# Kernel tuning notes

Measured on AMD Instinct MI355X. Metric: run time of the kernel, lower is better.

Reference implementation:

```python
import jax, jax.numpy as jnp
import numpy as np

H, W = 4096, 4096
KH, KW = 16, 16


def setup_inputs() -> dict:
    key = jax.random.key(0)
    kx, kw = jax.random.split(key)
    x = jax.random.normal(kx, (H, W), dtype=jnp.float32)
    weight = jax.random.normal(kw, (KH, KW), dtype=jnp.float32)
    bias = jnp.zeros((1,), dtype=jnp.float32)
    return {"x": x, "weight": weight, "bias": bias}


def reference(x, weight, bias):
    # 2D valid cross-correlation (no kernel flip), single channel, + scalar bias.
    # lax.conv_general_dilated computes cross-correlation by default.
    lhs = x[None, None, :, :]          # [1,1,H,W]
    rhs = weight[None, None, :, :]     # [1,1,KH,KW]
    y = jax.lax.conv_general_dilated(
        lhs, rhs,
        window_strides=(1, 1),
        padding="VALID",
        dimension_numbers=("NCHW", "OIHW", "NCHW"),
    )[0, 0]                            # [H-KH+1, W-KW+1]
    return y + bias[0]
```

## Files before the change

kernel.cpp:

```cpp
#include <hip/hip_runtime.h>

#define IH 4096
#define IW 4096
#define KH 16
#define KW 16
#define OH 4081
#define OW 4081

#define TBR 64
#define TBC 128
#define LROWS 79
#define LSTR 168

typedef short bf16x8 __attribute__((ext_vector_type(8)));
typedef float f32x16 __attribute__((ext_vector_type(16)));

static __device__ __forceinline__ unsigned int f2bf(float f) {
    unsigned int u = __float_as_uint(f);
    return (u + 0x7FFFu + ((u >> 16) & 1u)) >> 16;
}

__global__ void build_B(const float* __restrict__ wgt, unsigned short* __restrict__ Bt) {
    int idx = blockIdx.x * 256 + threadIdx.x;
    if (idx >= 16 * 3 * 512) return;
    int j    = idx & 7;
    int lane = (idx >> 3) & 63;
    int n    = lane & 31;
    int hi   = lane >> 5;
    int c    = (idx >> 9) % 3;
    int u    = idx / 1536;
    int vp   = c * 16 + hi * 8 + j;
    int t    = vp - n;
    float val = (t >= 0 && t < KW) ? wgt[u * KW + t] : 0.0f;
    Bt[idx] = (unsigned short)f2bf(val);
}

__global__ __launch_bounds__(256, 6)
void conv_mfma32(const float* __restrict__ x,
                 const unsigned short* __restrict__ Bt,
                 const float* __restrict__ bias,
                 float* __restrict__ out) {
    __shared__ unsigned short tile[LROWS * LSTR];

    const int tid  = threadIdx.x;
    const int lane = tid & 63;
    const int wv   = tid >> 6;
    const int rb   = wv >> 1;
    const int cb   = wv & 1;
    const int m    = lane & 31;
    const int hi   = lane >> 5;
    const int gy0  = blockIdx.y * TBR;
    const int gx0  = blockIdx.x * TBC;

    for (int idx = tid; idx < LROWS * 18; idx += 256) {
        int row = idx / 18;
        int c   = idx - row * 18;
        int gy  = gy0 + row;
        int gx  = gx0 + 8 * c;
        float4 q0 = make_float4(0.f, 0.f, 0.f, 0.f);
        float4 q1 = q0;
        if (gy < IH && gx < IW) {
            q0 = *reinterpret_cast<const float4*>(x + (size_t)gy * IW + gx);
            q1 = *reinterpret_cast<const float4*>(x + (size_t)gy * IW + gx + 4);
        }
        uint4 p;
        p.x = f2bf(q0.x) | (f2bf(q0.y) << 16);
        p.y = f2bf(q0.z) | (f2bf(q0.w) << 16);
        p.z = f2bf(q1.x) | (f2bf(q1.y) << 16);
        p.w = f2bf(q1.z) | (f2bf(q1.w) << 16);
        *reinterpret_cast<uint4*>(&tile[row * LSTR + c * 8]) = p;
    }
    __syncthreads();

    f32x16 acc0 = {0,0,0,0,0,0,0,0,0,0,0,0,0,0,0,0};
    f32x16 acc1 = {0,0,0,0,0,0,0,0,0,0,0,0,0,0,0,0};

    const int cB = cb * 8 + hi;
    const unsigned short* Blane = Bt + lane * 8;

    bf16x8 bc0 = *reinterpret_cast<const bf16x8*>(Blane + 0);
    bf16x8 bc1 = *reinterpret_cast<const bf16x8*>(Blane + 512);
    bf16x8 bc2 = *reinterpret_cast<const bf16x8*>(Blane + 1024);

#pragma unroll
    for (int u = 0; u < KH; ++u) {
        bf16x8 bn0 = bc0, bn1 = bc1, bn2 = bc2;
        if (u + 1 < KH) {
            const unsigned short* Bu = Blane + (u + 1) * 1536;
            bn0 = *reinterpret_cast<const bf16x8*>(Bu + 0);
            bn1 = *reinterpret_cast<const bf16x8*>(Bu + 512);
            bn2 = *reinterpret_cast<const bf16x8*>(Bu + 1024);
        }

        const int rowA = rb * 32 + m + u;
        const unsigned short* rbase = &tile[rowA * LSTR];

        bf16x8 a0 = *reinterpret_cast<const bf16x8*>(rbase + (cB + 0) * 8);
        bf16x8 a1 = *reinterpret_cast<const bf16x8*>(rbase + (cB + 2) * 8);
        bf16x8 a2 = *reinterpret_cast<const bf16x8*>(rbase + (cB + 4) * 8);
        bf16x8 a3 = *reinterpret_cast<const bf16x8*>(rbase + (cB + 6) * 8);
        bf16x8 a4 = *reinterpret_cast<const bf16x8*>(rbase + (cB + 8) * 8);

        acc0 = __builtin_amdgcn_mfma_f32_32x32x16_bf16(a0, bc0, acc0, 0, 0, 0);
        acc0 = __builtin_amdgcn_mfma_f32_32x32x16_bf16(a1, bc1, acc0, 0, 0, 0);
        acc0 = __builtin_amdgcn_mfma_f32_32x32x16_bf16(a2, bc2, acc0, 0, 0, 0);
        acc1 = __builtin_amdgcn_mfma_f32_32x32x16_bf16(a2, bc0, acc1, 0, 0, 0);
        acc1 = __builtin_amdgcn_mfma_f32_32x32x16_bf16(a3, bc1, acc1, 0, 0, 0);
        acc1 = __builtin_amdgcn_mfma_f32_32x32x16_bf16(a4, bc2, acc1, 0, 0, 0);

        bc0 = bn0; bc1 = bn1; bc2 = bn2;
    }

    const float bv   = bias[0];
    const int   row0 = gy0 + rb * 32 + 4 * hi;
    const int   col0 = gx0 + cb * 64 + m;
    const bool  full = (gy0 + TBR <= OH) && (gx0 + TBC <= OW);

#pragma unroll
    for (int g = 0; g < 2; ++g) {
        const f32x16 acc = g ? acc1 : acc0;
        const int col = col0 + g * 32;
        float* op = out + col;
        if (full) {
#pragma unroll
            for (int r = 0; r < 16; ++r) {
                int rr = row0 + (r & 3) + 8 * (r >> 2);
                op[(size_t)rr * OW] = acc[r] + bv;
            }
        } else if (col < OW) {
#pragma unroll
            for (int r = 0; r < 16; ++r) {
                int rr = row0 + (r & 3) + 8 * (r >> 2);
                if (rr < OH) op[(size_t)rr * OW] = acc[r] + bv;
            }
        }
    }
}

extern "C" void kernel_launch(void* const* d_in, const int* in_sizes, int n_in,
                              void* d_out, int out_size, void* d_ws, size_t ws_size,
                              hipStream_t stream) {
    const float* x  = (const float*)d_in[0];
    const float* w  = (const float*)d_in[1];
    const float* b  = (const float*)d_in[2];
    float* out = (float*)d_out;
    unsigned short* Bt = (unsigned short*)d_ws;

    build_B<<<96, 256, 0, stream>>>(w, Bt);

    dim3 grid((OW + TBC - 1) / TBC, (OH + TBR - 1) / TBR);
    conv_mfma32<<<grid, dim3(256), 0, stream>>>(x, Bt, b, out);
}
```

Measured before the change: 137.3 us.

## Stream row strips through an LDS ring buffer with register-staged prefetch

Each block now walks four 64-row output strips down a 128-column stripe instead of computing one 64x128 tile. Input rows go through a 144-row LDS ring. Each step prefetches the next 64 rows into registers while the MFMA loop runs, then converts them and writes them to LDS. This cuts the repeated 15-row halo reload and bf16 conversion between vertically adjacent tiles and overlaps global loads with compute. In exchange it uses 512-thread blocks with one accumulator per wave, far fewer blocks, and extra register pressure from the staged prefetch data.

```diff
diff --git a/kernel.cpp b/kernel.cpp
--- a/kernel.cpp
+++ b/kernel.cpp
@@ -7,10 +7,12 @@
 #define OH 4081
 #define OW 4081
 
-#define TBR 64
 #define TBC 128
-#define LROWS 79
+#define STEP 64
+#define NSTEP 4
+#define RING 144
 #define LSTR 168
+#define CHW 18
 
 typedef short bf16x8 __attribute__((ext_vector_type(8)));
 typedef float f32x16 __attribute__((ext_vector_type(16)));
@@ -35,27 +37,27 @@
     Bt[idx] = (unsigned short)f2bf(val);
 }
 
-__global__ __launch_bounds__(256, 6)
-void conv_mfma32(const float* __restrict__ x,
-                 const unsigned short* __restrict__ Bt,
-                 const float* __restrict__ bias,
-                 float* __restrict__ out) {
-    __shared__ unsigned short tile[LROWS * LSTR];
+__global__ __launch_bounds__(512, 4)
+void conv_pipe(const float* __restrict__ x,
+               const unsigned short* __restrict__ Bt,
+               const float* __restrict__ bias,
+               float* __restrict__ out) {
+    __shared__ unsigned short ring[RING * LSTR];
 
     const int tid  = threadIdx.x;
     const int lane = tid & 63;
     const int wv   = tid >> 6;
-    const int rb   = wv >> 1;
-    const int cb   = wv & 1;
+    const int rb   = wv & 1;
+    const int cb   = wv >> 1;
     const int m    = lane & 31;
     const int hi   = lane >> 5;
-    const int gy0  = blockIdx.y * TBR;
     const int gx0  = blockIdx.x * TBC;
+    const int oy0  = blockIdx.y * (STEP * NSTEP);
 
-    for (int idx = tid; idx < LROWS * 18; idx += 256) {
-        int row = idx / 18;
-        int c   = idx - row * 18;
-        int gy  = gy0 + row;
+    for (int idx = tid; idx < 80 * CHW; idx += 512) {
+        int row = idx / CHW;
+        int c   = idx - row * CHW;
+        int gy  = oy0 + row;
         int gx  = gx0 + 8 * c;
         float4 q0 = make_float4(0.f, 0.f, 0.f, 0.f);
         float4 q1 = q0;
@@ -68,72 +70,101 @@
         p.y = f2bf(q0.z) | (f2bf(q0.w) << 16);
         p.z = f2bf(q1.x) | (f2bf(q1.y) << 16);
         p.w = f2bf(q1.z) | (f2bf(q1.w) << 16);
-        *reinterpret_cast<uint4*>(&tile[row * LSTR + c * 8]) = p;
+        *reinterpret_cast<uint4*>(&ring[row * LSTR + c * 8]) = p;
     }
     __syncthreads();
 
-    f32x16 acc0 = {0,0,0,0,0,0,0,0,0,0,0,0,0,0,0,0};
-    f32x16 acc1 = {0,0,0,0,0,0,0,0,0,0,0,0,0,0,0,0};
+    const unsigned short* Blane = Bt + lane * 8;
+    const int  cA = 4 * cb + hi;
+    const float bv = bias[0];
 
-    const int cB = cb * 8 + hi;
-    const unsigned short* Blane = Bt + lane * 8;
+    for (int s = 0; s < NSTEP; ++s) {
+        float4 p0[3], p1[3];
+        int pring[3], pcc[3];
+        bool pval[3];
+        if (s + 1 < NSTEP) {
+#pragma unroll
+            for (int k = 0; k < 3; ++k) {
+                int idx  = tid + k * 512;
+                bool v   = idx < STEP * CHW;
+                int row  = idx / CHW;
+                int c    = idx - row * CHW;
+                int woff = 64 * s + 80 + row;
+                int rr   = woff - (woff >= RING ? RING : 0);
+                int gy   = oy0 + woff;
+                int gx   = gx0 + 8 * c;
+                pring[k] = rr; pcc[k] = c; pval[k] = v;
+                float4 q0 = make_float4(0.f, 0.f, 0.f, 0.f);
+                float4 q1 = q0;
+                if (v && gy < IH && gx < IW) {
+                    q0 = *reinterpret_cast<const float4*>(x + (size_t)gy * IW + gx);
+                    q1 = *reinterpret_cast<const float4*>(x + (size_t)gy * IW + gx + 4);
+                }
+                p0[k] = q0; p1[k] = q1;
+            }
+        }
 
-    bf16x8 bc0 = *reinterpret_cast<const bf16x8*>(Blane + 0);
-    bf16x8 bc1 = *reinterpret_cast<const bf16x8*>(Blane + 512);
-    bf16x8 bc2 = *reinterpret_cast<const bf16x8*>(Blane + 1024);
+        f32x16 acc = {0,0,0,0,0,0,0,0,0,0,0,0,0,0,0,0};
+        bf16x8 bc0 = *reinterpret_cast<const bf16x8*>(Blane + 0);
+        bf16x8 bc1 = *reinterpret_cast<const bf16x8*>(Blane + 512);
+        bf16x8 bc2 = *reinterpret_cast<const bf16x8*>(Blane + 1024);
 
 #pragma unroll
-    for (int u = 0; u < KH; ++u) {
-        bf16x8 bn0 = bc0, bn1 = bc1, bn2 = bc2;
-        if (u + 1 < KH) {
-            const unsigned short* Bu = Blane + (u + 1) * 1536;
-            bn0 = *reinterpret_cast<const bf16x8*>(Bu + 0);
-            bn1 = *reinterpret_cast<const bf16x8*>(Bu + 512);
-            bn2 = *reinterpret_cast<const bf16x8*>(Bu + 1024);
+        for (int u = 0; u < KH; ++u) {
+            bf16x8 bn0 = bc0, bn1 = bc1, bn2 = bc2;
+            if (u + 1 < KH) {
+                const unsigned short* Bu = Blane + (u + 1) * 1536;
+                bn0 = *reinterpret_cast<const bf16x8*>(Bu + 0);
+                bn1 = *reinterpret_cast<const bf16x8*>(Bu + 512);
+                bn2 = *reinterpret_cast<const bf16x8*>(Bu + 1024);
+            }
+            int off = 64 * s + 32 * rb + m + u;
+            int rr  = off - (off >= RING ? RING : 0);
+            const unsigned short* rbase = &ring[rr * LSTR];
+            bf16x8 a0 = *reinterpret_cast<const bf16x8*>(rbase + (cA + 0) * 8);
+            bf16x8 a1 = *reinterpret_cast<const bf16x8*>(rbase + (cA + 2) * 8);
+            bf16x8 a2 = *reinterpret_cast<const bf16x8*>(rbase + (cA + 4) * 8);
+            acc = __builtin_amdgcn_mfma_f32_32x32x16_bf16(a0, bc0, acc, 0, 0, 0);
+            acc = __builtin_amdgcn_mfma_f32_32x32x16_bf16(a1, bc1, acc, 0, 0, 0);
+            acc = __builtin_amdgcn_mfma_f32_32x32x16_bf16(a2, bc2, acc, 0, 0, 0);
+            bc0 = bn0; bc1 = bn1; bc2 = bn2;
         }
 
-        const int rowA = rb * 32 + m + u;
-        const unsigned short* rbase = &tile[rowA * LSTR];
-
-        bf16x8 a0 = *reinterpret_cast<const bf16x8*>(rbase + (cB + 0) * 8);
-        bf16x8 a1 = *reinterpret_cast<const bf16x8*>(rbase + (cB + 2) * 8);
-        bf16x8 a2 = *reinterpret_cast<const bf16x8*>(rbase + (cB + 4) * 8);
-        bf16x8 a3 = *reinterpret_cast<const bf16x8*>(rbase + (cB + 6) * 8);
-        bf16x8 a4 = *reinterpret_cast<const bf16x8*>(rbase + (cB + 8) * 8);
-
-        acc0 = __builtin_amdgcn_mfma_f32_32x32x16_bf16(a0, bc0, acc0, 0, 0, 0);
-        acc0 = __builtin_amdgcn_mfma_f32_32x32x16_bf16(a1, bc1, acc0, 0, 0, 0);
-        acc0 = __builtin_amdgcn_mfma_f32_32x32x16_bf16(a2, bc2, acc0, 0, 0, 0);
-        acc1 = __builtin_amdgcn_mfma_f32_32x32x16_bf16(a2, bc0, acc1, 0, 0, 0);
-        acc1 = __builtin_amdgcn_mfma_f32_32x32x16_bf16(a3, bc1, acc1, 0, 0, 0);
-        acc1 = __builtin_amdgcn_mfma_f32_32x32x16_bf16(a4, bc2, acc1, 0, 0, 0);
-
-        bc0 = bn0; bc1 = bn1; bc2 = bn2;
-    }
-
-    const float bv   = bias[0];
-    const int   row0 = gy0 + rb * 32 + 4 * hi;
-    const int   col0 = gx0 + cb * 64 + m;
-    const bool  full = (gy0 + TBR <= OH) && (gx0 + TBC <= OW);
-
+        if (s + 1 < NSTEP) {
 #pragma unroll
-    for (int g = 0; g < 2; ++g) {
-        const f32x16 acc = g ? acc1 : acc0;
-        const int col = col0 + g * 32;
-        float* op = out + col;
-        if (full) {
-#pragma unroll
-            for (int r = 0; r < 16; ++r) {
-                int rr = row0 + (r & 3) + 8 * (r >> 2);
-                op[(size_t)rr * OW] = acc[r] + bv;
-            }
-        } else if (col < OW) {
-#pragma unroll
-            for (int r = 0; r < 16; ++r) {
-                int rr = row0 + (r & 3) + 8 * (r >> 2);
-                if (rr < OH) op[(size_t)rr * OW] = acc[r] + bv;
+            for (int k = 0; k < 3; ++k) {
+                if (pval[k]) {
+                    uint4 p;
+                    p.x = f2bf(p0[k].x) | (f2bf(p0[k].y) << 16);
+                    p.y = f2bf(p0[k].z) | (f2bf(p0[k].w) << 16);
+                    p.z = f2bf(p1[k].x) | (f2bf(p1[k].y) << 16);
+                    p.w = f2bf(p1[k].z) | (f2bf(p1[k].w) << 16);
+                    *reinterpret_cast<uint4*>(&ring[pring[k] * LSTR + pcc[k] * 8]) = p;
+                }
             }
         }
+
+        {
+            const int row0 = oy0 + 64 * s + 32 * rb + 4 * hi;
+            const int col  = gx0 + 32 * cb + m;
+            const bool full = (oy0 + 64 * s + 64 <= OH) && (gx0 + TBC <= OW);
+            float* op = out + col;
+            if (full) {
+#pragma unroll
+                for (int r = 0; r < 16; ++r) {
+                    int rr = row0 + (r & 3) + 8 * (r >> 2);
+                    op[(size_t)rr * OW] = acc[r] + bv;
+                }
+            } else if (col < OW) {
+#pragma unroll
+                for (int r = 0; r < 16; ++r) {
+                    int rr = row0 + (r & 3) + 8 * (r >> 2);
+                    if (rr < OH) op[(size_t)rr * OW] = acc[r] + bv;
+                }
+            }
+        }
+
+        __syncthreads();
     }
 }
 
@@ -148,6 +179,7 @@
 
     build_B<<<96, 256, 0, stream>>>(w, Bt);
 
-    dim3 grid((OW + TBC - 1) / TBC, (OH + TBR - 1) / TBR);
-    conv_mfma32<<<grid, dim3(256), 0, stream>>>(x, Bt, b, out);
+    dim3 grid((OW + TBC - 1) / TBC,
+              (OH + STEP * NSTEP - 1) / (STEP * NSTEP));
+    conv_pipe<<<grid, dim3(512), 0, stream>>>(x, Bt, b, out);
 }
```

After: 308.3 us. +124.6%, slower.
